# Performance work log

Hardware: AMD Instinct MI355X
Metric: run time of the kernel (lower is better)

Reference implementation:

```python
import jax, jax.numpy as jnp
import numpy as np

N_POINTS = 1 << 20
N_LEVELS = 16
F_PER_LVL = 2
LOG2_T = 19
T = 1 << LOG2_T
BASE_RES = 16
PER_LEVEL_SCALE = float(np.exp2(np.log2(2048.0 / 16.0) / (N_LEVELS - 1)))
# 8 trilinear corner offsets [8,3]
OFFSETS = np.stack(np.meshgrid(*([np.array([0, 1])] * 3), indexing='ij'), axis=-1).reshape(8, 3)
PRIMES = np.array([1, 2654435761, 805459861], dtype=np.uint32)  # tcnn spatial hash primes


def _level_params(l):
    # tcnn: grid_scale = 2^(l*log2(s)) * base - 1 ; resolution = ceil(scale)+1
    scale = np.exp2(l * np.log2(PER_LEVEL_SCALE)) * BASE_RES - 1.0
    res = int(np.ceil(scale)) + 1
    return float(scale), res


def hash_encode(x, table):
    """x: [N,3] in [0,1]; table: [L,T,F]. Returns [N, L*F]."""
    offs = jnp.asarray(OFFSETS)                     # [8,3] int32
    primes = jnp.asarray(PRIMES)                    # [3] uint32
    feats = []
    for l in range(N_LEVELS):
        scale, res = _level_params(l)
        pos = x * scale + 0.5                       # [N,3]
        pos_grid = jnp.floor(pos)
        w = pos - pos_grid                          # [N,3] interp weights
        c0 = pos_grid.astype(jnp.int32)             # [N,3]
        corners = c0[None, :, :] + offs[:, None, :]  # [8,N,3]
        if res ** 3 <= T:
            # dense indexing for coarse levels (fits in hashmap)
            cc = jnp.clip(corners, 0, res - 1)
            idx = cc[..., 0] + cc[..., 1] * res + cc[..., 2] * (res * res)
        else:
            cu = corners.astype(jnp.uint32)
            h = (cu[..., 0] * primes[0]) ^ (cu[..., 1] * primes[1]) ^ (cu[..., 2] * primes[2])
            idx = (h & jnp.uint32(T - 1)).astype(jnp.int32)
        f = table[l][idx]                           # [8,N,F] gather
        # trilinear weights: prod over dims of (w if corner bit else 1-w)
        wc = jnp.prod(jnp.where(offs[:, None, :] == 1, w[None], 1.0 - w[None]), axis=-1)  # [8,N]
        feats.append(jnp.sum(wc[..., None] * f, axis=0))  # [N,F]
    return jnp.concatenate(feats, axis=-1)          # [N, 32]


def _softplus10(z):
    return jax.nn.softplus(10.0 * z) / 10.0


def setup_inputs() -> dict:
    key = jax.random.key(0)
    k = jax.random.split(key, 6)
    x = jax.random.uniform(k[0], (N_POINTS, 3), dtype=jnp.float32)
    table = jax.random.normal(k[1], (N_LEVELS, T, F_PER_LVL), dtype=jnp.float32) * 1e-2
    w1 = jax.random.normal(k[2], (64, 32), dtype=jnp.float32) * 0.1
    w2 = jax.random.normal(k[3], (64, 64), dtype=jnp.float32) * 0.1
    w3 = jax.random.normal(k[4], (64, 64), dtype=jnp.float32) * 0.1
    w4 = jax.random.normal(k[5], (1, 64), dtype=jnp.float32) * 0.1
    return {"x": x, "table": table, "w1": w1, "w2": w2, "w3": w3, "w4": w4}


def reference(x, table, w1, w2, w3, w4):
    enc = hash_encode(x, table)                     # [N,32]
    h = _softplus10(enc @ w1.T)
    h = _softplus10(h @ w2.T)
    h = _softplus10(h @ w3.T)
    sdf = h @ w4.T                                  # [N,1]
    return sdf
```

## Files before the change

### kernel.cpp

```cpp
#include <hip/hip_runtime.h>
#include <cmath>

#define T_SIZE (1u << 19)
#define CB 512
#define NBLK 128
#define RCAP 3584

typedef _Float16 h8 __attribute__((ext_vector_type(8)));
typedef _Float16 h4 __attribute__((ext_vector_type(4)));
typedef _Float16 h2 __attribute__((ext_vector_type(2)));
typedef float f4 __attribute__((ext_vector_type(4)));

struct Levels {
    float scale[16];
    int   res[16];
    unsigned dense_mask;
};

__device__ __forceinline__ float softplus10(float z) {
    float e = __builtin_amdgcn_exp2f(fminf(z * 14.426950408889634f, 126.0f));
    return __builtin_amdgcn_logf(1.0f + e) * 0.069314718055994531f;
}

__device__ __forceinline__ unsigned spread3(unsigned v) {
    v &= 1023u;
    v = (v | (v << 16)) & 0x030000FFu;
    v = (v | (v << 8))  & 0x0300F00Fu;
    v = (v | (v << 4))  & 0x030C30C3u;
    v = (v | (v << 2))  & 0x09249249u;
    return v;
}

__device__ __forceinline__ unsigned morton_key(float px, float py, float pz) {
    unsigned qx = (unsigned)fminf(fmaxf(px, 0.f) * 32.f, 31.f);
    unsigned qy = (unsigned)fminf(fmaxf(py, 0.f) * 32.f, 31.f);
    unsigned qz = (unsigned)fminf(fmaxf(pz, 0.f) * 32.f, 31.f);
    return (spread3(qx) << 2) | (spread3(qy) << 1) | spread3(qz);
}

__global__ __launch_bounds__(256) void convert_kernel(
    const float2* __restrict__ t, h2* __restrict__ o, int total4,
    const float* __restrict__ w1, const float* __restrict__ w2,
    const float* __restrict__ w3, _Float16* __restrict__ wh,
    const float* __restrict__ xs, unsigned* __restrict__ M, int N)
{
    const int histStart = (total4 + 10240 + 255) >> 8;
    if ((int)blockIdx.x >= histStart) {
        __shared__ unsigned h[CB];
        const int blk = blockIdx.x - histStart;
        for (int t2 = threadIdx.x; t2 < CB; t2 += 256) h[t2] = 0u;
        __syncthreads();
        const int per = N / NBLK;
        const int s = blk * per;
        for (int i = s + threadIdx.x; i < s + per; i += 256) {
            unsigned k = morton_key(xs[3 * i], xs[3 * i + 1], xs[3 * i + 2]) >> 6;
            atomicAdd(&h[k], 1u);
        }
        __syncthreads();
        for (int t2 = threadIdx.x; t2 < CB; t2 += 256)
            M[t2 * NBLK + blk] = h[t2];
        return;
    }
    int i = blockIdx.x * 256 + threadIdx.x;
    if (i < total4) {
        const float2* src = t + (size_t)i * 4;
        h8 r;
#pragma unroll
        for (int j = 0; j < 4; ++j) {
            float2 v = src[j];
            r[2 * j]     = (_Float16)v.x;
            r[2 * j + 1] = (_Float16)v.y;
        }
        *(h8*)(o + (size_t)i * 4) = r;
    } else {
        int k = i - total4;
        if (k < 10240) {
            float v = (k < 2048) ? w1[k] : (k < 6144) ? w2[k - 2048] : w3[k - 6144];
            wh[k] = (_Float16)v;
        }
    }
}

__global__ __launch_bounds__(1024) void scan_kernel(
    const unsigned* __restrict__ M, unsigned* __restrict__ Ms)
{
    __shared__ unsigned tmp[1024];
    const int t = threadIdx.x;
    const int PER = (CB * NBLK) / 1024;
    unsigned s = 0;
    for (int j = 0; j < PER; ++j) s += M[t * PER + j];
    tmp[t] = s;
    __syncthreads();
    for (int d = 1; d < 1024; d <<= 1) {
        unsigned v = (t >= d) ? tmp[t - d] : 0u;
        __syncthreads();
        tmp[t] += v;
        __syncthreads();
    }
    unsigned run = (t > 0) ? tmp[t - 1] : 0u;
    for (int j = 0; j < PER; ++j) {
        unsigned v = M[t * PER + j];
        Ms[t * PER + j] = run;
        run += v;
    }
}

__global__ __launch_bounds__(256) void cscatter_kernel(
    const float* __restrict__ xs, const unsigned* __restrict__ Ms,
    float4* __restrict__ sx4, int N)
{
    __shared__ unsigned cur[CB];
    for (int t = threadIdx.x; t < CB; t += 256)
        cur[t] = Ms[t * NBLK + blockIdx.x];
    __syncthreads();
    const int per = N / NBLK;
    const int s = blockIdx.x * per;
    for (int i = s + threadIdx.x; i < s + per; i += 256) {
        float px = xs[3 * i], py = xs[3 * i + 1], pz = xs[3 * i + 2];
        unsigned k = morton_key(px, py, pz) >> 6;
        unsigned pos = atomicAdd(&cur[k], 1u);
        sx4[pos] = make_float4(px, py, pz, __uint_as_float((unsigned)i));
    }
}

__global__ __launch_bounds__(256) void refine_kernel(
    float4* __restrict__ sx4, const unsigned* __restrict__ Ms, int N)
{
    __shared__ float4 pts[RCAP];
    __shared__ unsigned h[64], base[64];
    const int b = blockIdx.x;
    const unsigned s = Ms[b * NBLK];
    const unsigned e = (b == CB - 1) ? (unsigned)N : Ms[(b + 1) * NBLK];
    const unsigned cnt = e - s;
    if (cnt > RCAP) return;
    if (threadIdx.x < 64) h[threadIdx.x] = 0u;
    __syncthreads();
    for (unsigned i = threadIdx.x; i < cnt; i += 256) {
        float4 q = sx4[s + i];
        pts[i] = q;
        unsigned k = morton_key(q.x, q.y, q.z) & 63u;
        atomicAdd(&h[k], 1u);
    }
    __syncthreads();
    if (threadIdx.x == 0) {
        unsigned a = 0;
        for (int j = 0; j < 64; ++j) { base[j] = a; a += h[j]; }
    }
    __syncthreads();
    if (threadIdx.x < 64) h[threadIdx.x] = 0u;
    __syncthreads();
    for (unsigned i = threadIdx.x; i < cnt; i += 256) {
        float4 q = pts[i];
        unsigned k = morton_key(q.x, q.y, q.z) & 63u;
        unsigned r = base[k] + atomicAdd(&h[k], 1u);
        sx4[s + r] = q;
    }
}

__device__ __forceinline__ void gather_pair(
    const h2* __restrict__ tl, unsigned i0, unsigned i1,
    float2& v0, float2& v1)
{
    unsigned g = i0 & ~3u;
    union { h8 v; uint4 u; } cv;
    cv.v = *(const h8*)(tl + g);
    unsigned p0 = i0 & 3u;
    unsigned a01 = (p0 & 1u) ? cv.u.y : cv.u.x;
    unsigned a23 = (p0 & 1u) ? cv.u.w : cv.u.z;
    unsigned e0  = (p0 & 2u) ? a23 : a01;
    unsigned e1;
    if ((i1 & ~3u) == g) {
        unsigned p1 = i1 & 3u;
        unsigned b01 = (p1 & 1u) ? cv.u.y : cv.u.x;
        unsigned b23 = (p1 & 1u) ? cv.u.w : cv.u.z;
        e1 = (p1 & 2u) ? b23 : b01;
    } else {
        e1 = *(const unsigned*)(tl + i1);
    }
    h2 c0 = __builtin_bit_cast(h2, e0);
    h2 c1 = __builtin_bit_cast(h2, e1);
    v0 = make_float2((float)c0[0], (float)c0[1]);
    v1 = make_float2((float)c1[0], (float)c1[1]);
}

__device__ __forceinline__ h2 encode_point(
    float px, float py, float pz, float s, int res, bool dense,
    const h2* __restrict__ tl)
{
    float fx = px * s + 0.5f, fy = py * s + 0.5f, fz = pz * s + 0.5f;
    float gx = floorf(fx), gy = floorf(fy), gz = floorf(fz);
    float wx = fx - gx, wy = fy - gy, wz = fz - gz;
    int cx = (int)gx, cy = (int)gy, cz = (int)gz;

    float2 vx0[4], vx1[4];
    if (dense) {
        int r1 = res - 1;
        int x0 = min(cx, r1), x1 = min(cx + 1, r1);
        int y0 = min(cy, r1), y1 = min(cy + 1, r1);
        int z0 = min(cz, r1), z1 = min(cz + 1, r1);
        int rr = res * res;
        int bases[4] = {y0 * res + z0 * rr, y0 * res + z1 * rr,
                        y1 * res + z0 * rr, y1 * res + z1 * rr};
#pragma unroll
        for (int j = 0; j < 4; ++j)
            gather_pair(tl, (unsigned)(x0 + bases[j]), (unsigned)(x1 + bases[j]),
                        vx0[j], vx1[j]);
    } else {
        unsigned hy0 = (unsigned)cy * 2654435761u, hy1 = (unsigned)(cy + 1) * 2654435761u;
        unsigned hz0 = (unsigned)cz * 805459861u,  hz1 = (unsigned)(cz + 1) * 805459861u;
        unsigned Y[4] = {hy0 ^ hz0, hy0 ^ hz1, hy1 ^ hz0, hy1 ^ hz1};
        const unsigned M = T_SIZE - 1;
#pragma unroll
        for (int j = 0; j < 4; ++j)
            gather_pair(tl, ((unsigned)cx ^ Y[j]) & M,
                        ((unsigned)(cx + 1) ^ Y[j]) & M, vx0[j], vx1[j]);
    }

    float wx0 = 1.f - wx, wy0 = 1.f - wy, wz0 = 1.f - wz;
    float wyz[4] = {wy0 * wz0, wy0 * wz, wy * wz0, wy * wz};
    float f0 = 0.f, f1 = 0.f;
#pragma unroll
    for (int j = 0; j < 4; ++j) {
        float w0 = wx0 * wyz[j], w1 = wx * wyz[j];
        f0 += w0 * vx0[j].x + w1 * vx1[j].x;
        f1 += w0 * vx0[j].y + w1 * vx1[j].y;
    }
    h2 r; r[0] = (_Float16)f0; r[1] = (_Float16)f1;
    return r;
}

__global__ __launch_bounds__(256) void encode_kernel(
    const float* __restrict__ xs, const h2* __restrict__ table,
    h2* __restrict__ enc2, Levels lv, int lbase, int N)
{
    __shared__ float sx[768];
    const int i0 = blockIdx.x * 256;
    for (int t = threadIdx.x; t < 768; t += 256) sx[t] = xs[(size_t)i0 * 3 + t];
    __syncthreads();

    const int l = lbase + blockIdx.y;
    const int i = i0 + threadIdx.x;
    if (i >= N) return;
    h2 r = encode_point(sx[threadIdx.x * 3], sx[threadIdx.x * 3 + 1],
                        sx[threadIdx.x * 3 + 2], lv.scale[l], lv.res[l],
                        (lv.dense_mask >> l) & 1u, table + (size_t)l * T_SIZE);
    enc2[(size_t)l * N + i] = r;
}

__global__ __launch_bounds__(256) void encode_kernel_sorted(
    const float4* __restrict__ xs4, const h2* __restrict__ table,
    h2* __restrict__ enc2, Levels lv, int lbase, int N)
{
    const int i = blockIdx.x * 256 + threadIdx.x;
    if (i >= N) return;
    const int l = lbase + blockIdx.y;
    float4 q = xs4[i];
    h2 r = encode_point(q.x, q.y, q.z, lv.scale[l], lv.res[l],
                        (lv.dense_mask >> l) & 1u, table + (size_t)l * T_SIZE);
    enc2[(size_t)l * N + i] = r;
}

template <typename WT>
__device__ __forceinline__ h8 load_frag8(const WT* p) {
    if constexpr (sizeof(WT) == 2) {
        return *(const h8*)p;
    } else {
        h8 r;
#pragma unroll
        for (int j = 0; j < 8; ++j) r[j] = (_Float16)p[j];
        return r;
    }
}

template <typename WT, bool LOCAL, bool SORTED>
__global__ __launch_bounds__(256, 3) void fused_kernel(
    const float* __restrict__ xs, const float4* __restrict__ xs4,
    const h2* __restrict__ table16, const h2* __restrict__ enc2,
    const WT* __restrict__ w1, const WT* __restrict__ w2,
    const WT* __restrict__ w3, const float* __restrict__ w4,
    float* __restrict__ out, Levels lv, int N)
{
    constexpr int AR = 72;
    __shared__ __align__(16) char smem[4 * 9216];
    __shared__ float sx[768];

    const int tid  = threadIdx.x;
    const int wave = tid >> 6;
    const int lane = tid & 63;
    const int lrow = lane & 15;
    const int quad = lane >> 4;
    const int base = blockIdx.x * 256;
    char* wmem = smem + wave * 9216;
    const f4 zero = {0.f, 0.f, 0.f, 0.f};

    float px, py, pz;
    unsigned oi = 0;
    if constexpr (SORTED) {
        float4 q = xs4[base + tid];
        px = q.x; py = q.y; pz = q.z;
        oi = __float_as_uint(q.w);
    } else {
        for (int t = tid; t < 768; t += 256) sx[t] = xs[(size_t)base * 3 + t];
        __syncthreads();
        px = sx[tid * 3]; py = sx[tid * 3 + 1]; pz = sx[tid * 3 + 2];
    }
    const int p = tid & 63;

    if (LOCAL) {
#pragma unroll
        for (int l = 10; l < 15; ++l) {
            h2 v = enc2[(size_t)l * N + base + tid];
            *(h2*)(wmem + ((l >> 2) << 10) + (p << 4) + ((l & 3) << 2)) = v;
        }
        const int LMAP[11] = {15, 5, 6, 7, 8, 9, 0, 1, 2, 3, 4};
#pragma unroll
        for (int s6 = 0; s6 < 11; ++s6) {
            const int l = LMAP[s6];
            h2 v = encode_point(px, py, pz, lv.scale[l], lv.res[l],
                                (lv.dense_mask >> l) & 1u,
                                table16 + (size_t)l * T_SIZE);
            *(h2*)(wmem + ((l >> 2) << 10) + (p << 4) + ((l & 3) << 2)) = v;
        }
    } else {
#pragma unroll
        for (int l = 0; l < 16; ++l) {
            h2 v = enc2[(size_t)l * N + base + tid];
            *(h2*)(wmem + ((l >> 2) << 10) + (p << 4) + ((l & 3) << 2)) = v;
        }
    }

    asm volatile("" ::: "memory");

    h8 aW1[4];
#pragma unroll
    for (int tm = 0; tm < 4; ++tm)
        aW1[tm] = load_frag8(w1 + (tm * 16 + lrow) * 32 + quad * 8);
    h8 aW2[4][2], aW3[4][2];
#pragma unroll
    for (int tm = 0; tm < 4; ++tm)
#pragma unroll
        for (int km = 0; km < 2; ++km) {
            aW2[tm][km] = load_frag8(w2 + (tm * 16 + lrow) * 64 + km * 32 + quad * 8);
            aW3[tm][km] = load_frag8(w3 + (tm * 16 + lrow) * 64 + km * 32 + quad * 8);
        }
    h4 w4q[4];
#pragma unroll
    for (int tm = 0; tm < 4; ++tm)
#pragma unroll
        for (int r = 0; r < 4; ++r) w4q[tm][r] = (_Float16)w4[tm * 16 + quad * 4 + r];

    h8 bin[4];
#pragma unroll
    for (int t = 0; t < 4; ++t)
        bin[t] = *(const h8*)(wmem + (quad << 10) + ((t * 16 + lrow) << 4));

    _Float16* wAct = (_Float16*)wmem;

#pragma unroll
    for (int t = 0; t < 4; ++t) {
        const int arow = (t * 16 + lrow) * AR;
#pragma unroll
        for (int tm = 0; tm < 4; ++tm) {
            f4 acc = __builtin_amdgcn_mfma_f32_16x16x32_f16(aW1[tm], bin[t], zero, 0, 0, 0);
            h4 pk;
#pragma unroll
            for (int r = 0; r < 4; ++r) pk[r] = (_Float16)softplus10(acc[r]);
            *(h4*)&wAct[arow + tm * 16 + quad * 4] = pk;
        }
    }

#pragma unroll
    for (int t = 0; t < 4; ++t) {
        const int arow = (t * 16 + lrow) * AR;
        h8 b0 = *(const h8*)&wAct[arow + quad * 8];
        h8 b1 = *(const h8*)&wAct[arow + 32 + quad * 8];
        f4 accs[4];
#pragma unroll
        for (int tm = 0; tm < 4; ++tm) {
            f4 acc = __builtin_amdgcn_mfma_f32_16x16x32_f16(aW2[tm][0], b0, zero, 0, 0, 0);
            acc     = __builtin_amdgcn_mfma_f32_16x16x32_f16(aW2[tm][1], b1, acc,  0, 0, 0);
            accs[tm] = acc;
        }
#pragma unroll
        for (int tm = 0; tm < 4; ++tm) {
            h4 pk;
#pragma unroll
            for (int r = 0; r < 4; ++r) pk[r] = (_Float16)softplus10(accs[tm][r]);
            *(h4*)&wAct[arow + tm * 16 + quad * 4] = pk;
        }
    }

#pragma unroll
    for (int t = 0; t < 4; ++t) {
        const int arow = (t * 16 + lrow) * AR;
        h8 b0 = *(const h8*)&wAct[arow + quad * 8];
        h8 b1 = *(const h8*)&wAct[arow + 32 + quad * 8];
        float sum = 0.f;
#pragma unroll
        for (int tm = 0; tm < 4; ++tm) {
            f4 acc = __builtin_amdgcn_mfma_f32_16x16x32_f16(aW3[tm][0], b0, zero, 0, 0, 0);
            acc     = __builtin_amdgcn_mfma_f32_16x16x32_f16(aW3[tm][1], b1, acc,  0, 0, 0);
#pragma unroll
            for (int r = 0; r < 4; ++r)
                sum += (float)w4q[tm][r] * softplus10(acc[r]);
        }
        sum += __shfl_xor(sum, 16, 64);
        sum += __shfl_xor(sum, 32, 64);
        if constexpr (SORTED) {
            unsigned t_oi = __shfl(oi, t * 16 + lrow, 64);
            if (quad == 0) out[t_oi] = sum;
        } else {
            if (quad == 0)
                out[base + wave * 64 + t * 16 + lrow] = sum;
        }
    }
}

__global__ __launch_bounds__(256) void encode_kernel_f32(
    const float* __restrict__ xs, const float2* __restrict__ table,
    h2* __restrict__ enc2, Levels lv, int N)
{
    const int i = blockIdx.x * 256 + threadIdx.x;
    const int l = blockIdx.y;
    if (i >= N) return;
    float px = xs[3 * i], py = xs[3 * i + 1], pz = xs[3 * i + 2];
    float s = lv.scale[l];
    int res = lv.res[l];
    float fx = px * s + 0.5f, fy = py * s + 0.5f, fz = pz * s + 0.5f;
    float gx = floorf(fx), gy = floorf(fy), gz = floorf(fz);
    float wx = fx - gx, wy = fy - gy, wz = fz - gz;
    int cx = (int)gx, cy = (int)gy, cz = (int)gz;
    unsigned idx[8];
    if ((lv.dense_mask >> l) & 1u) {
        int r1 = res - 1;
        int x0 = min(cx, r1), x1 = min(cx + 1, r1);
        int y0 = min(cy, r1), y1 = min(cy + 1, r1);
        int z0 = min(cz, r1), z1 = min(cz + 1, r1);
        int rr = res * res;
        idx[0] = x0 + y0 * res + z0 * rr; idx[1] = x0 + y0 * res + z1 * rr;
        idx[2] = x0 + y1 * res + z0 * rr; idx[3] = x0 + y1 * res + z1 * rr;
        idx[4] = x1 + y0 * res + z0 * rr; idx[5] = x1 + y0 * res + z1 * rr;
        idx[6] = x1 + y1 * res + z0 * rr; idx[7] = x1 + y1 * res + z1 * rr;
    } else {
        unsigned hx0 = (unsigned)cx, hx1 = (unsigned)(cx + 1);
        unsigned hy0 = (unsigned)cy * 2654435761u, hy1 = (unsigned)(cy + 1) * 2654435761u;
        unsigned hz0 = (unsigned)cz * 805459861u,  hz1 = (unsigned)(cz + 1) * 805459861u;
        idx[0] = (hx0^hy0^hz0) & (T_SIZE-1); idx[1] = (hx0^hy0^hz1) & (T_SIZE-1);
        idx[2] = (hx0^hy1^hz0) & (T_SIZE-1); idx[3] = (hx0^hy1^hz1) & (T_SIZE-1);
        idx[4] = (hx1^hy0^hz0) & (T_SIZE-1); idx[5] = (hx1^hy0^hz1) & (T_SIZE-1);
        idx[6] = (hx1^hy1^hz0) & (T_SIZE-1); idx[7] = (hx1^hy1^hz1) & (T_SIZE-1);
    }
    const float2* tl = table + (size_t)l * T_SIZE;
    float wx0 = 1.f - wx, wy0 = 1.f - wy, wz0 = 1.f - wz;
    float wcs[8] = {wx0*wy0*wz0, wx0*wy0*wz, wx0*wy*wz0, wx0*wy*wz,
                    wx*wy0*wz0,  wx*wy0*wz,  wx*wy*wz0,  wx*wy*wz};
    float f0 = 0.f, f1 = 0.f;
#pragma unroll
    for (int c = 0; c < 8; ++c) {
        float2 v = tl[idx[c]];
        f0 += wcs[c] * v.x; f1 += wcs[c] * v.y;
    }
    h2 r; r[0] = (_Float16)f0; r[1] = (_Float16)f1;
    enc2[(size_t)l * N + i] = r;
}

extern "C" void kernel_launch(void* const* d_in, const int* in_sizes, int n_in,
                              void* d_out, int out_size, void* d_ws, size_t ws_size,
                              hipStream_t stream) {
    const float* x     = (const float*)d_in[0];
    const float* table = (const float*)d_in[1];
    const float* w1    = (const float*)d_in[2];
    const float* w2    = (const float*)d_in[3];
    const float* w3    = (const float*)d_in[4];
    const float* w4    = (const float*)d_in[5];
    float* out = (float*)d_out;
    const int N = in_sizes[0] / 3;

    Levels lv;
    lv.dense_mask = 0;
    const double pls = exp2(log2(2048.0 / 16.0) / 15.0);
    const double lg  = log2(pls);
    for (int l = 0; l < 16; ++l) {
        double sc = exp2((double)l * lg) * 16.0 - 1.0;
        int res = (int)ceil(sc) + 1;
        lv.scale[l] = (float)sc;
        lv.res[l]   = res;
        if ((long long)res * res * res <= (long long)T_SIZE) lv.dense_mask |= (1u << l);
    }

    const size_t encBytes   = (size_t)16 * N * 4;
    const size_t tableBytes = (size_t)16 * T_SIZE * 4;
    const size_t whBytes    = 32768;
    const size_t sx4Bytes   = (size_t)N * 16;
    h2* enc2 = (h2*)d_ws;

    const int ptBlocks = (N + 255) / 256;

    if (ws_size >= encBytes + tableBytes + whBytes + sx4Bytes
        && N == NBLK * 8192) {
        h2* table16    = (h2*)((char*)d_ws + encBytes);
        _Float16* wh   = (_Float16*)((char*)d_ws + encBytes + tableBytes);
        float4* sx4    = (float4*)((char*)d_ws + encBytes + tableBytes + whBytes);
        unsigned* M  = (unsigned*)d_ws;
        unsigned* Ms = (unsigned*)((char*)d_ws + 512 * 1024);

        const int total4 = 16 * T_SIZE / 4;
        const int convBlocks = (total4 + 10240 + 255) / 256;
        hipLaunchKernelGGL(convert_kernel, dim3(convBlocks + NBLK), dim3(256), 0,
                           stream, (const float2*)table, table16, total4,
                           w1, w2, w3, wh, x, M, N);
        hipLaunchKernelGGL(scan_kernel, dim3(1), dim3(1024), 0, stream, M, Ms);
        hipLaunchKernelGGL(cscatter_kernel, dim3(NBLK), dim3(256), 0, stream,
                           x, Ms, sx4, N);
        hipLaunchKernelGGL(refine_kernel, dim3(CB), dim3(256), 0, stream,
                           sx4, Ms, N);

        hipLaunchKernelGGL(encode_kernel_sorted, dim3(ptBlocks, 5), dim3(256),
                           0, stream, (const float4*)sx4, (const h2*)table16,
                           enc2, lv, 10, N);
        hipLaunchKernelGGL((fused_kernel<_Float16, true, true>), dim3(ptBlocks), dim3(256),
                           0, stream, x, (const float4*)sx4, (const h2*)table16,
                           (const h2*)enc2, wh, wh + 2048, wh + 6144, w4, out, lv, N);
    } else if (ws_size >= encBytes + tableBytes + whBytes) {
        h2* table16 = (h2*)((char*)d_ws + encBytes);
        _Float16* wh = (_Float16*)((char*)d_ws + encBytes + tableBytes);
        const int total4 = 16 * T_SIZE / 4;
        const int convBlocks = (total4 + 10240 + 255) / 256;
        hipLaunchKernelGGL(convert_kernel, dim3(convBlocks), dim3(256), 0, stream,
                           (const float2*)table, table16, total4, w1, w2, w3, wh,
                           x, (unsigned*)nullptr, N);
        hipLaunchKernelGGL(encode_kernel, dim3(ptBlocks, 5), dim3(256), 0, stream,
                           x, (const h2*)table16, enc2, lv, 10, N);
        hipLaunchKernelGGL((fused_kernel<_Float16, true, false>), dim3(ptBlocks), dim3(256),
                           0, stream, x, (const float4*)nullptr, (const h2*)table16,
                           (const h2*)enc2, wh, wh + 2048, wh + 6144, w4, out, lv, N);
    } else {
        hipLaunchKernelGGL(encode_kernel_f32, dim3(ptBlocks, 16), dim3(256), 0, stream,
                           x, (const float2*)table, enc2, lv, N);
        hipLaunchKernelGGL((fused_kernel<float, false, false>), dim3(ptBlocks), dim3(256),
                           0, stream, x, (const float4*)nullptr, (const h2*)nullptr,
                           (const h2*)enc2, w1, w2, w3, w4, out, lv, N);
    }
}
```

Measured before the change: 450.6 us.

## Fuse all hash-grid levels into the MLP kernel, drop separate encode pass

Removes the separate encode_kernel_sorted pass for levels 10-14 and encodes all 16 levels inside the fused MLP kernel, packing four levels per 16-byte LDS store. Level 15 and the other fine groups are encoded first. This drops the enc2 round trip through global memory and one kernel launch. In exchange, fine-level gather latency now sits on the fused kernel's critical path, where it may be harder to hide at the occupancy set by launch_bounds(256,3). Workspace layout is rearranged, and the f32 fallback gets its own staged kernel.

```diff
diff --git a/kernel.cpp b/kernel.cpp
--- a/kernel.cpp
+++ b/kernel.cpp
@@ -229,55 +229,12 @@
     return r;
 }
 
-__global__ __launch_bounds__(256) void encode_kernel(
-    const float* __restrict__ xs, const h2* __restrict__ table,
-    h2* __restrict__ enc2, Levels lv, int lbase, int N)
-{
-    __shared__ float sx[768];
-    const int i0 = blockIdx.x * 256;
-    for (int t = threadIdx.x; t < 768; t += 256) sx[t] = xs[(size_t)i0 * 3 + t];
-    __syncthreads();
-
-    const int l = lbase + blockIdx.y;
-    const int i = i0 + threadIdx.x;
-    if (i >= N) return;
-    h2 r = encode_point(sx[threadIdx.x * 3], sx[threadIdx.x * 3 + 1],
-                        sx[threadIdx.x * 3 + 2], lv.scale[l], lv.res[l],
-                        (lv.dense_mask >> l) & 1u, table + (size_t)l * T_SIZE);
-    enc2[(size_t)l * N + i] = r;
-}
-
-__global__ __launch_bounds__(256) void encode_kernel_sorted(
-    const float4* __restrict__ xs4, const h2* __restrict__ table,
-    h2* __restrict__ enc2, Levels lv, int lbase, int N)
-{
-    const int i = blockIdx.x * 256 + threadIdx.x;
-    if (i >= N) return;
-    const int l = lbase + blockIdx.y;
-    float4 q = xs4[i];
-    h2 r = encode_point(q.x, q.y, q.z, lv.scale[l], lv.res[l],
-                        (lv.dense_mask >> l) & 1u, table + (size_t)l * T_SIZE);
-    enc2[(size_t)l * N + i] = r;
-}
-
-template <typename WT>
-__device__ __forceinline__ h8 load_frag8(const WT* p) {
-    if constexpr (sizeof(WT) == 2) {
-        return *(const h8*)p;
-    } else {
-        h8 r;
-#pragma unroll
-        for (int j = 0; j < 8; ++j) r[j] = (_Float16)p[j];
-        return r;
-    }
-}
-
-template <typename WT, bool LOCAL, bool SORTED>
-__global__ __launch_bounds__(256, 3) void fused_kernel(
+template <bool SORTED>
+__global__ __launch_bounds__(256, 3) void fused_all_kernel(
     const float* __restrict__ xs, const float4* __restrict__ xs4,
-    const h2* __restrict__ table16, const h2* __restrict__ enc2,
-    const WT* __restrict__ w1, const WT* __restrict__ w2,
-    const WT* __restrict__ w3, const float* __restrict__ w4,
+    const h2* __restrict__ table16,
+    const _Float16* __restrict__ w1, const _Float16* __restrict__ w2,
+    const _Float16* __restrict__ w3, const float* __restrict__ w4,
     float* __restrict__ out, Levels lv, int N)
 {
     constexpr int AR = 72;
@@ -306,27 +263,21 @@
     }
     const int p = tid & 63;
 
-    if (LOCAL) {
-#pragma unroll
-        for (int l = 10; l < 15; ++l) {
-            h2 v = enc2[(size_t)l * N + base + tid];
-            *(h2*)(wmem + ((l >> 2) << 10) + (p << 4) + ((l & 3) << 2)) = v;
-        }
-        const int LMAP[11] = {15, 5, 6, 7, 8, 9, 0, 1, 2, 3, 4};
-#pragma unroll
-        for (int s6 = 0; s6 < 11; ++s6) {
-            const int l = LMAP[s6];
+    const int GORD[4] = {3, 2, 1, 0};
+#pragma unroll
+    for (int gi = 0; gi < 4; ++gi) {
+        const int g = GORD[gi];
+        h8 pack;
+#pragma unroll
+        for (int s4 = 0; s4 < 4; ++s4) {
+            const int l = g * 4 + ((g == 3) ? ((s4 + 3) & 3) : s4);
             h2 v = encode_point(px, py, pz, lv.scale[l], lv.res[l],
                                 (lv.dense_mask >> l) & 1u,
                                 table16 + (size_t)l * T_SIZE);
-            *(h2*)(wmem + ((l >> 2) << 10) + (p << 4) + ((l & 3) << 2)) = v;
-        }
-    } else {
-#pragma unroll
-        for (int l = 0; l < 16; ++l) {
-            h2 v = enc2[(size_t)l * N + base + tid];
-            *(h2*)(wmem + ((l >> 2) << 10) + (p << 4) + ((l & 3) << 2)) = v;
-        }
+            pack[2 * (l & 3)]     = v[0];
+            pack[2 * (l & 3) + 1] = v[1];
+        }
+        *(h8*)(wmem + (g << 10) + (p << 4)) = pack;
     }
 
     asm volatile("" ::: "memory");
@@ -334,14 +285,14 @@
     h8 aW1[4];
 #pragma unroll
     for (int tm = 0; tm < 4; ++tm)
-        aW1[tm] = load_frag8(w1 + (tm * 16 + lrow) * 32 + quad * 8);
+        aW1[tm] = *(const h8*)(w1 + (tm * 16 + lrow) * 32 + quad * 8);
     h8 aW2[4][2], aW3[4][2];
 #pragma unroll
     for (int tm = 0; tm < 4; ++tm)
 #pragma unroll
         for (int km = 0; km < 2; ++km) {
-            aW2[tm][km] = load_frag8(w2 + (tm * 16 + lrow) * 64 + km * 32 + quad * 8);
-            aW3[tm][km] = load_frag8(w3 + (tm * 16 + lrow) * 64 + km * 32 + quad * 8);
+            aW2[tm][km] = *(const h8*)(w2 + (tm * 16 + lrow) * 64 + km * 32 + quad * 8);
+            aW3[tm][km] = *(const h8*)(w3 + (tm * 16 + lrow) * 64 + km * 32 + quad * 8);
         }
     h4 w4q[4];
 #pragma unroll
@@ -464,6 +415,114 @@
     enc2[(size_t)l * N + i] = r;
 }
 
+__global__ __launch_bounds__(256, 3) void fused_staged_f32(
+    const h2* __restrict__ enc2,
+    const float* __restrict__ w1, const float* __restrict__ w2,
+    const float* __restrict__ w3, const float* __restrict__ w4,
+    float* __restrict__ out, int N)
+{
+    constexpr int AR = 72;
+    __shared__ __align__(16) char smem[4 * 9216];
+    const int tid  = threadIdx.x;
+    const int wave = tid >> 6;
+    const int lane = tid & 63;
+    const int lrow = lane & 15;
+    const int quad = lane >> 4;
+    const int base = blockIdx.x * 256;
+    char* wmem = smem + wave * 9216;
+    const f4 zero = {0.f, 0.f, 0.f, 0.f};
+    const int p = tid & 63;
+#pragma unroll
+    for (int l = 0; l < 16; ++l) {
+        h2 v = enc2[(size_t)l * N + base + tid];
+        *(h2*)(wmem + ((l >> 2) << 10) + (p << 4) + ((l & 3) << 2)) = v;
+    }
+    asm volatile("" ::: "memory");
+    h8 aW1[4];
+#pragma unroll
+    for (int tm = 0; tm < 4; ++tm) {
+        h8 r;
+#pragma unroll
+        for (int j = 0; j < 8; ++j)
+            r[j] = (_Float16)w1[(tm * 16 + lrow) * 32 + quad * 8 + j];
+        aW1[tm] = r;
+    }
+    h8 aW2[4][2], aW3[4][2];
+#pragma unroll
+    for (int tm = 0; tm < 4; ++tm)
+#pragma unroll
+        for (int km = 0; km < 2; ++km) {
+            h8 r2, r3;
+#pragma unroll
+            for (int j = 0; j < 8; ++j) {
+                r2[j] = (_Float16)w2[(tm * 16 + lrow) * 64 + km * 32 + quad * 8 + j];
+                r3[j] = (_Float16)w3[(tm * 16 + lrow) * 64 + km * 32 + quad * 8 + j];
+            }
+            aW2[tm][km] = r2; aW3[tm][km] = r3;
+        }
+    h4 w4q[4];
+#pragma unroll
+    for (int tm = 0; tm < 4; ++tm)
+#pragma unroll
+        for (int r = 0; r < 4; ++r) w4q[tm][r] = (_Float16)w4[tm * 16 + quad * 4 + r];
+    h8 bin[4];
+#pragma unroll
+    for (int t = 0; t < 4; ++t)
+        bin[t] = *(const h8*)(wmem + (quad << 10) + ((t * 16 + lrow) << 4));
+    _Float16* wAct = (_Float16*)wmem;
+#pragma unroll
+    for (int t = 0; t < 4; ++t) {
+        const int arow = (t * 16 + lrow) * AR;
+#pragma unroll
+        for (int tm = 0; tm < 4; ++tm) {
+            f4 acc = __builtin_amdgcn_mfma_f32_16x16x32_f16(aW1[tm], bin[t], zero, 0, 0, 0);
+            h4 pk;
+#pragma unroll
+            for (int r = 0; r < 4; ++r) pk[r] = (_Float16)softplus10(acc[r]);
+            *(h4*)&wAct[arow + tm * 16 + quad * 4] = pk;
+        }
+    }
+#pragma unroll
+    for (int t = 0; t < 4; ++t) {
+        const int arow = (t * 16 + lrow) * AR;
+        h8 b0 = *(const h8*)&wAct[arow + quad * 8];
+        h8 b1 = *(const h8*)&wAct[arow + 32 + quad * 8];
+        f4 accs[4];
+#pragma unroll
+        for (int tm = 0; tm < 4; ++tm) {
+            f4 acc = __builtin_amdgcn_mfma_f32_16x16x32_f16(aW2[tm][0], b0, zero, 0, 0, 0);
+            acc     = __builtin_amdgcn_mfma_f32_16x16x32_f16(aW2[tm][1], b1, acc,  0, 0, 0);
+            accs[tm] = acc;
+        }
+#pragma unroll
+        for (int tm = 0; tm < 4; ++tm) {
+            h4 pk;
+#pragma unroll
+            for (int r = 0; r < 4; ++r) pk[r] = (_Float16)softplus10(accs[tm][r]);
+            *(h4*)&wAct[arow + tm * 16 + quad * 4] = pk;
+        }
+    }
+#pragma unroll
+    for (int t = 0; t < 4; ++t) {
+        const int arow = (t * 16 + lrow) * AR;
+        h8 b0 = *(const h8*)&wAct[arow + quad * 8];
+        h8 b1 = *(const h8*)&wAct[arow + 32 + quad * 8];
+        float sum = 0.f;
+#pragma unroll
+        for (int tm = 0; tm < 4; ++tm) {
+            f4 acc = __builtin_amdgcn_mfma_f32_16x16x32_f16(aW3[tm][0], b0, zero, 0, 0, 0);
+            acc     = __builtin_amdgcn_mfma_f32_16x16x32_f16(aW3[tm][1], b1, acc,  0, 0, 0);
+#pragma unroll
+            for (int r = 0; r < 4; ++r)
+                sum += (float)w4q[tm][r] * softplus10(acc[r]);
+        }
+        sum += __shfl_xor(sum, 16, 64);
+        sum += __shfl_xor(sum, 32, 64);
+        if (quad == 0)
+            out[base + wave * 64 + t * 16 + lrow] = sum;
+    }
+}
+
 extern "C" void kernel_launch(void* const* d_in, const int* in_sizes, int n_in,
                               void* d_out, int out_size, void* d_ws, size_t ws_size,
                               hipStream_t stream) {
@@ -488,24 +547,23 @@
         if ((long long)res * res * res <= (long long)T_SIZE) lv.dense_mask |= (1u << l);
     }
 
-    const size_t encBytes   = (size_t)16 * N * 4;
     const size_t tableBytes = (size_t)16 * T_SIZE * 4;
     const size_t whBytes    = 32768;
     const size_t sx4Bytes   = (size_t)N * 16;
-    h2* enc2 = (h2*)d_ws;
+    const size_t mBytes     = (size_t)CB * NBLK * 4;
 
     const int ptBlocks = (N + 255) / 256;
-
-    if (ws_size >= encBytes + tableBytes + whBytes + sx4Bytes
+    const int total4 = 16 * T_SIZE / 4;
+    const int convBlocks = (total4 + 10240 + 255) / 256;
+
+    if (ws_size >= tableBytes + whBytes + sx4Bytes + 2 * mBytes
         && N == NBLK * 8192) {
-        h2* table16    = (h2*)((char*)d_ws + encBytes);
-        _Float16* wh   = (_Float16*)((char*)d_ws + encBytes + tableBytes);
-        float4* sx4    = (float4*)((char*)d_ws + encBytes + tableBytes + whBytes);
-        unsigned* M  = (unsigned*)d_ws;
-        unsigned* Ms = (unsigned*)((char*)d_ws + 512 * 1024);
-
-        const int total4 = 16 * T_SIZE / 4;
-        const int convBlocks = (total4 + 10240 + 255) / 256;
+        h2* table16    = (h2*)d_ws;
+        _Float16* wh   = (_Float16*)((char*)d_ws + tableBytes);
+        float4* sx4    = (float4*)((char*)d_ws + tableBytes + whBytes);
+        unsigned* M    = (unsigned*)((char*)d_ws + tableBytes + whBytes + sx4Bytes);
+        unsigned* Ms   = M + (size_t)CB * NBLK;
+
         hipLaunchKernelGGL(convert_kernel, dim3(convBlocks + NBLK), dim3(256), 0,
                            stream, (const float2*)table, table16, total4,
                            w1, w2, w3, wh, x, M, N);
@@ -515,30 +573,23 @@
         hipLaunchKernelGGL(refine_kernel, dim3(CB), dim3(256), 0, stream,
                            sx4, Ms, N);
 
-        hipLaunchKernelGGL(encode_kernel_sorted, dim3(ptBlocks, 5), dim3(256),
-                           0, stream, (const float4*)sx4, (const h2*)table16,
-                           enc2, lv, 10, N);
-        hipLaunchKernelGGL((fused_kernel<_Float16, true, true>), dim3(ptBlocks), dim3(256),
+        hipLaunchKernelGGL((fused_all_kernel<true>), dim3(ptBlocks), dim3(256),
                            0, stream, x, (const float4*)sx4, (const h2*)table16,
-                           (const h2*)enc2, wh, wh + 2048, wh + 6144, w4, out, lv, N);
-    } else if (ws_size >= encBytes + tableBytes + whBytes) {
-        h2* table16 = (h2*)((char*)d_ws + encBytes);
-        _Float16* wh = (_Float16*)((char*)d_ws + encBytes + tableBytes);
-        const int total4 = 16 * T_SIZE / 4;
-        const int convBlocks = (total4 + 10240 + 255) / 256;
+                           wh, wh + 2048, wh + 6144, w4, out, lv, N);
+    } else if (ws_size >= tableBytes + whBytes) {
+        h2* table16 = (h2*)d_ws;
+        _Float16* wh = (_Float16*)((char*)d_ws + tableBytes);
         hipLaunchKernelGGL(convert_kernel, dim3(convBlocks), dim3(256), 0, stream,
                            (const float2*)table, table16, total4, w1, w2, w3, wh,
                            x, (unsigned*)nullptr, N);
-        hipLaunchKernelGGL(encode_kernel, dim3(ptBlocks, 5), dim3(256), 0, stream,
-                           x, (const h2*)table16, enc2, lv, 10, N);
-        hipLaunchKernelGGL((fused_kernel<_Float16, true, false>), dim3(ptBlocks), dim3(256),
+        hipLaunchKernelGGL((fused_all_kernel<false>), dim3(ptBlocks), dim3(256),
                            0, stream, x, (const float4*)nullptr, (const h2*)table16,
-                           (const h2*)enc2, wh, wh + 2048, wh + 6144, w4, out, lv, N);
+                           wh, wh + 2048, wh + 6144, w4, out, lv, N);
     } else {
+        h2* enc2 = (h2*)d_ws;
         hipLaunchKernelGGL(encode_kernel_f32, dim3(ptBlocks, 16), dim3(256), 0, stream,
                            x, (const float2*)table, enc2, lv, N);
-        hipLaunchKernelGGL((fused_kernel<float, false, false>), dim3(ptBlocks), dim3(256),
-                           0, stream, x, (const float4*)nullptr, (const h2*)nullptr,
-                           (const h2*)enc2, w1, w2, w3, w4, out, lv, N);
-    }
-}
+        hipLaunchKernelGGL(fused_staged_f32, dim3(ptBlocks), dim3(256),
+                           0, stream, (const h2*)enc2, w1, w2, w3, w4, out, N);
+    }
+}
```

Result: slower. 519.7 us (+15.3%).
